# Kernel tuning notes

Hardware: AMD Instinct MI355X
Metric: run time of the kernel (lower is better)

Reference implementation:

```python
import jax, jax.numpy as jnp
import numpy as np

DIM = 768
HEADS = 12
EXPERTS = 8
HID = 3072  # dim * moe_mlp_ratio(=4)
TOP_K = 2
LN_EPS = 1e-5


def _layer_norm(x, g, b):
    mu = x.mean(-1, keepdims=True)
    var = ((x - mu) ** 2).mean(-1, keepdims=True)
    return (x - mu) * jax.lax.rsqrt(var + LN_EPS) * g + b


def setup_inputs() -> dict:
    key = jax.random.key(0)
    ks = jax.random.split(key, 16)
    s = 0.02
    return {
        "x": jax.random.normal(ks[0], (8, 196, DIM), jnp.float32),
        "ln1_g": jnp.ones((DIM,), jnp.float32),
        "ln1_b": jnp.zeros((DIM,), jnp.float32),
        "qkv_w": jax.random.normal(ks[1], (DIM, 3 * DIM), jnp.float32) * s,
        "qkv_b": jnp.zeros((3 * DIM,), jnp.float32),
        "proj_w": jax.random.normal(ks[2], (DIM, DIM), jnp.float32) * s,
        "proj_b": jnp.zeros((DIM,), jnp.float32),
        "ln2_g": jnp.ones((DIM,), jnp.float32),
        "ln2_b": jnp.zeros((DIM,), jnp.float32),
        "gate_w": jax.random.normal(ks[3], (DIM, EXPERTS), jnp.float32) * s,
        "w1": jax.random.normal(ks[4], (EXPERTS, DIM, HID), jnp.float32) * s,
        "b1": jnp.zeros((EXPERTS, HID), jnp.float32),
        "w2": jax.random.normal(ks[5], (EXPERTS, HID, DIM), jnp.float32) * s,
        "b2": jnp.zeros((EXPERTS, DIM), jnp.float32),
    }


def _attention(x, qkv_w, qkv_b, proj_w, proj_b):
    B, N, C = x.shape
    hd = C // HEADS
    qkv = (x @ qkv_w + qkv_b).reshape(B, N, 3, HEADS, hd).transpose(2, 0, 3, 1, 4)
    q, k, v = qkv[0], qkv[1], qkv[2]  # [B,H,N,hd]
    attn = jax.nn.softmax(jnp.einsum("bhnd,bhmd->bhnm", q, k) * (hd ** -0.5), axis=-1)
    o = jnp.einsum("bhnm,bhmd->bhnd", attn, v).transpose(0, 2, 1, 3).reshape(B, N, C)
    return o @ proj_w + proj_b


def _moe_mlp(xn, gate_w, w1, b1, w2, b2):
    # xn: [T, D]; noisy top-k gate in eval mode (no noise)
    T = xn.shape[0]
    logits = xn @ gate_w                                   # [T, E]
    top_logits, top_idx = jax.lax.top_k(logits, TOP_K)     # [T, k]
    top_gates = jax.nn.softmax(top_logits, axis=-1)        # [T, k]
    gates = jnp.zeros((T, EXPERTS), xn.dtype).at[
        jnp.arange(T)[:, None], top_idx
    ].set(top_gates)                                       # [T, E] sparse combine weights
    # dense-masked expert compute (math identical to dispatch: gate=0 tokens contribute 0)
    h = jax.nn.gelu(jnp.einsum("td,edh->teh", xn, w1) + b1, approximate=False)
    y = jnp.einsum("teh,ehd->ted", h, w2) + b2             # [T, E, D]
    return jnp.einsum("ted,te->td", y, gates)


def reference(x, ln1_g, ln1_b, qkv_w, qkv_b, proj_w, proj_b,
              ln2_g, ln2_b, gate_w, w1, b1, w2, b2):
    B, N, C = x.shape
    x = x + _attention(_layer_norm(x, ln1_g, ln1_b), qkv_w, qkv_b, proj_w, proj_b)
    xn = _layer_norm(x, ln2_g, ln2_b).reshape(B * N, C)
    moe_out = _moe_mlp(xn, gate_w, w1, b1, w2, b2).reshape(B, N, C)
    return x + moe_out
```

## Files before the change

### kernel.cpp

```cpp
#include <hip/hip_runtime.h>
#include <hip/hip_bf16.h>
#include <math.h>

#define DIMC 768
#define HEADS 12
#define HD 64
#define EXPERTS 8
#define HID 3072
#define BB 8
#define NN 196
#define TT (BB*NN)
#define CAP_ROWS 4224
#define LN_EPS 1e-5f

typedef float f32x4_t __attribute__((ext_vector_type(4)));
typedef short bf16x8_t __attribute__((ext_vector_type(8)));
typedef unsigned short u16x8_t __attribute__((ext_vector_type(8)));

__device__ __forceinline__ unsigned short f2bf(float f) {
    unsigned int u = __float_as_uint(f);
    u += 0x7FFFu + ((u >> 16) & 1u);
    return (unsigned short)(u >> 16);
}
__device__ __forceinline__ float bf2f(unsigned short u) {
    return __uint_as_float(((unsigned int)u) << 16);
}

__device__ __forceinline__ void gl_lds16(const void* g, void* l) {
    __builtin_amdgcn_global_load_lds(
        (const __attribute__((address_space(1))) unsigned int*)g,
        (__attribute__((address_space(3))) unsigned int*)l, 16, 0, 0);
}

__device__ __forceinline__ int xcd_remap(int pbid, int nwg) {
    int q = nwg >> 3, r8 = nwg & 7;
    int xcd = pbid & 7, slot = pbid >> 3;
    return (xcd < r8) ? xcd * (q + 1) + slot
                      : r8 * (q + 1) + (xcd - r8) * q + slot;
}

template<int GATE>
__global__ void ln_kernel_t(const float* __restrict__ x, const float* __restrict__ g,
                            const float* __restrict__ b,
                            unsigned short* __restrict__ out_hi,
                            unsigned short* __restrict__ out_lo,
                            const float* __restrict__ gw, int* __restrict__ tok_e,
                            float* __restrict__ tok_g, int* __restrict__ counts) {
    int t = blockIdx.x;
    const float* xr = x + (size_t)t * DIMC;
    int tid = threadIdx.x;
    int lane = tid & 63, w = tid >> 6;
    float v0 = xr[tid], v1 = xr[tid + 256], v2 = xr[tid + 512];
    __shared__ float ws[4], vs[4];

    float s = v0 + v1 + v2;
    #pragma unroll
    for (int off = 32; off > 0; off >>= 1) s += __shfl_xor(s, off, 64);
    if (lane == 0) ws[w] = s;
    __syncthreads();
    float mu = (ws[0] + ws[1] + ws[2] + ws[3]) * (1.0f / DIMC);

    float d0 = v0 - mu, d1 = v1 - mu, d2 = v2 - mu;
    float q = d0 * d0 + d1 * d1 + d2 * d2;
    #pragma unroll
    for (int off = 32; off > 0; off >>= 1) q += __shfl_xor(q, off, 64);
    if (lane == 0) vs[w] = q;
    __syncthreads();
    float rstd = rsqrtf((vs[0] + vs[1] + vs[2] + vs[3]) * (1.0f / DIMC) + LN_EPS);

    float o0 = d0 * rstd * g[tid]       + b[tid];
    float o1 = d1 * rstd * g[tid + 256] + b[tid + 256];
    float o2 = d2 * rstd * g[tid + 512] + b[tid + 512];
    {
        unsigned short* o = out_hi + (size_t)t * DIMC;
        unsigned short h0 = f2bf(o0), h1 = f2bf(o1), h2 = f2bf(o2);
        o[tid] = h0; o[tid + 256] = h1; o[tid + 512] = h2;
        if (out_lo) {
            unsigned short* ol = out_lo + (size_t)t * DIMC;
            ol[tid]       = f2bf(o0 - bf2f(h0));
            ol[tid + 256] = f2bf(o1 - bf2f(h1));
            ol[tid + 512] = f2bf(o2 - bf2f(h2));
        }
    }
    if (GATE) {
        float p[8];
        const float* g0r = gw + (size_t)tid * 8;
        const float* g1r = gw + ((size_t)tid + 256) * 8;
        const float* g2r = gw + ((size_t)tid + 512) * 8;
        #pragma unroll
        for (int e = 0; e < 8; ++e)
            p[e] = o0 * g0r[e] + o1 * g1r[e] + o2 * g2r[e];
        #pragma unroll
        for (int off = 32; off > 0; off >>= 1)
            #pragma unroll
            for (int e = 0; e < 8; ++e) p[e] += __shfl_xor(p[e], off, 64);
        __shared__ float redw[4][8];
        if (lane == 0) {
            #pragma unroll
            for (int e = 0; e < 8; ++e) redw[w][e] = p[e];
        }
        __syncthreads();
        if (tid == 0) {
            float lg[8];
            #pragma unroll
            for (int e = 0; e < 8; ++e)
                lg[e] = redw[0][e] + redw[1][e] + redw[2][e] + redw[3][e];
            int e0 = 0; float l0 = lg[0];
            #pragma unroll
            for (int e = 1; e < 8; ++e) if (lg[e] > l0) { l0 = lg[e]; e0 = e; }
            int e1 = -1; float l1 = -3e38f;
            #pragma unroll
            for (int e = 0; e < 8; ++e) if (e != e0 && lg[e] > l1) { l1 = lg[e]; e1 = e; }
            float pp = expf(l1 - l0);
            float ga = 1.f / (1.f + pp);
            float gb = pp / (1.f + pp);
            tok_e[t*2] = e0; tok_e[t*2+1] = e1;
            tok_g[t*2] = ga; tok_g[t*2+1] = gb;
            atomicAdd(&counts[e0], 1);
            atomicAdd(&counts[e1], 1);
        }
    }
}

__global__ void attn_mfma_kernel(const float* __restrict__ qkv,
                                 unsigned short* __restrict__ ao_h,
                                 unsigned short* __restrict__ ao_l) {
    __shared__ char psb[64 * 896];
    __shared__ unsigned short QsH[64 * 64], QsL[64 * 64];
    __shared__ unsigned short KsH[64 * 64], KsL[64 * 64];

    int bh = blockIdx.x;
    int b = bh / HEADS, h = bh % HEADS;
    int q0 = blockIdx.y * 64;
    const float* base = qkv + (size_t)b * NN * 2304 + h * 64;

    int tid = threadIdx.x;
    int sr = tid >> 3, sq = tid & 7;
    int lane = tid & 63;
    int wid = tid >> 6;
    int wm = (wid >> 2) * 32;
    int wn = (wid & 3) * 16;
    int lrow = lane & 15;
    int lq = lane >> 4;
    int colb_base = lq * 16;

    {
        int r = sr;
        int n = q0 + r;
        float v[8] = {0.f,0.f,0.f,0.f,0.f,0.f,0.f,0.f};
        if (n < NN) {
            float4 a0 = *(const float4*)(base + (size_t)n * 2304 + sq * 8);
            float4 a1 = *(const float4*)(base + (size_t)n * 2304 + sq * 8 + 4);
            v[0]=a0.x; v[1]=a0.y; v[2]=a0.z; v[3]=a0.w;
            v[4]=a1.x; v[5]=a1.y; v[6]=a1.z; v[7]=a1.w;
        }
        u16x8_t hv, lv;
        #pragma unroll
        for (int t = 0; t < 8; ++t) {
            unsigned short hh = f2bf(v[t]);
            hv[t] = hh; lv[t] = f2bf(v[t] - bf2f(hh));
        }
        int off = r * 128 + ((sq * 16) ^ ((r & 7) << 4));
        *(u16x8_t*)((char*)QsH + off) = hv;
        *(u16x8_t*)((char*)QsL + off) = lv;
    }

    for (int kt = 0; kt < 4; ++kt) {
        int j0 = kt * 64;
        __syncthreads();
        {
            int r = sr;
            int n = j0 + r;
            float v[8] = {0.f,0.f,0.f,0.f,0.f,0.f,0.f,0.f};
            if (n < NN) {
                float4 a0 = *(const float4*)(base + (size_t)n * 2304 + 768 + sq * 8);
                float4 a1 = *(const float4*)(base + (size_t)n * 2304 + 768 + sq * 8 + 4);
                v[0]=a0.x; v[1]=a0.y; v[2]=a0.z; v[3]=a0.w;
                v[4]=a1.x; v[5]=a1.y; v[6]=a1.z; v[7]=a1.w;
            }
            u16x8_t hv, lv;
            #pragma unroll
            for (int t = 0; t < 8; ++t) {
                unsigned short hh = f2bf(v[t]);
                hv[t] = hh; lv[t] = f2bf(v[t] - bf2f(hh));
            }
            int off = r * 128 + ((sq * 16) ^ ((r & 7) << 4));
            *(u16x8_t*)((char*)KsH + off) = hv;
            *(u16x8_t*)((char*)KsL + off) = lv;
        }
        __syncthreads();

        f32x4_t acc[2] = {};
        #pragma unroll
        for (int kk = 0; kk < 2; ++kk) {
            int colb = kk * 64 + colb_base;
            bf16x8_t qh[2], ql[2], kh, kl;
            #pragma unroll
            for (int i = 0; i < 2; ++i) {
                int ra = wm + i * 16 + lrow;
                int oa = ra * 128 + (colb ^ ((ra & 7) << 4));
                qh[i] = *(const bf16x8_t*)((const char*)QsH + oa);
                ql[i] = *(const bf16x8_t*)((const char*)QsL + oa);
            }
            int rb = wn + lrow;
            int ob = rb * 128 + (colb ^ ((rb & 7) << 4));
            kh = *(const bf16x8_t*)((const char*)KsH + ob);
            kl = *(const bf16x8_t*)((const char*)KsL + ob);
            #pragma unroll
            for (int mi = 0; mi < 2; ++mi) {
                acc[mi] = __builtin_amdgcn_mfma_f32_16x16x32_bf16(qh[mi], kh, acc[mi], 0, 0, 0);
                acc[mi] = __builtin_amdgcn_mfma_f32_16x16x32_bf16(qh[mi], kl, acc[mi], 0, 0, 0);
                acc[mi] = __builtin_amdgcn_mfma_f32_16x16x32_bf16(ql[mi], kh, acc[mi], 0, 0, 0);
            }
        }
        int jc = j0 + wn + lrow;
        if (jc < 224) {
            #pragma unroll
            for (int mi = 0; mi < 2; ++mi) {
                #pragma unroll
                for (int j = 0; j < 4; ++j) {
                    int row = wm + mi * 16 + lq * 4 + j;
                    int s = (row & 7) ^ (row >> 3);
                    *(float*)(psb + row * 896 + ((jc * 4) ^ (s << 4))) = acc[mi][j] * 0.125f;
                }
            }
        }
    }
    __syncthreads();

    {
        int i = tid >> 3, l = tid & 7;
        int s = (i & 7) ^ (i >> 3);
        char* prow = psb + i * 896;
        float mx = -1e30f;
        for (int j = l; j < NN; j += 8) mx = fmaxf(mx, *(const float*)(prow + ((j * 4) ^ (s << 4))));
        mx = fmaxf(mx, __shfl_xor(mx, 1, 8));
        mx = fmaxf(mx, __shfl_xor(mx, 2, 8));
        mx = fmaxf(mx, __shfl_xor(mx, 4, 8));
        float sum = 0.f;
        for (int j = l; j < NN; j += 8) {
            float* pp = (float*)(prow + ((j * 4) ^ (s << 4)));
            float e = expf(*pp - mx); *pp = e; sum += e;
        }
        sum += __shfl_xor(sum, 1, 8);
        sum += __shfl_xor(sum, 2, 8);
        sum += __shfl_xor(sum, 4, 8);
        float inv = 1.f / sum;
        for (int j = l; j < NN; j += 8) {
            float* pp = (float*)(prow + ((j * 4) ^ (s << 4)));
            *pp *= inv;
        }
    }

    f32x4_t oacc[2] = {};
    for (int kt = 0; kt < 4; ++kt) {
        int j0 = kt * 64;
        __syncthreads();
        {
            int r = sr;
            int n = j0 + r;
            float v[8] = {0.f,0.f,0.f,0.f,0.f,0.f,0.f,0.f};
            if (n < NN) {
                float4 a0 = *(const float4*)(base + (size_t)n * 2304 + 1536 + sq * 8);
                float4 a1 = *(const float4*)(base + (size_t)n * 2304 + 1536 + sq * 8 + 4);
                v[0]=a0.x; v[1]=a0.y; v[2]=a0.z; v[3]=a0.w;
                v[4]=a1.x; v[5]=a1.y; v[6]=a1.z; v[7]=a1.w;
            }
            #pragma unroll
            for (int t = 0; t < 8; ++t) {
                int d = sq * 8 + t;
                int sw = ((d & 7) ^ (d >> 3)) << 4;
                unsigned short hh = f2bf(v[t]);
                int off = d * 128 + ((r * 2) ^ sw);
                *(unsigned short*)((char*)KsH + off) = hh;
                *(unsigned short*)((char*)KsL + off) = f2bf(v[t] - bf2f(hh));
            }
        }
        __syncthreads();

        int kkmax = (kt == 3) ? 1 : 2;
        for (int kk = 0; kk < kkmax; ++kk) {
            int colb = kk * 64 + colb_base;
            bf16x8_t pah[2], pal[2], vh, vl;
            #pragma unroll
            for (int i = 0; i < 2; ++i) {
                int ra = wm + i * 16 + lrow;
                int s = (ra & 7) ^ (ra >> 3);
                const char* prow = psb + ra * 896;
                int jb = (j0 + kk * 32 + lq * 8) * 4;
                float4 a0 = *(const float4*)(prow + (jb ^ (s << 4)));
                float4 a1 = *(const float4*)(prow + ((jb + 16) ^ (s << 4)));
                float vv[8] = {a0.x,a0.y,a0.z,a0.w,a1.x,a1.y,a1.z,a1.w};
                u16x8_t hv, lv;
                #pragma unroll
                for (int t = 0; t < 8; ++t) {
                    unsigned short hh = f2bf(vv[t]);
                    hv[t] = hh; lv[t] = f2bf(vv[t] - bf2f(hh));
                }
                pah[i] = *(bf16x8_t*)&hv;
                pal[i] = *(bf16x8_t*)&lv;
            }
            int rb = wn + lrow;
            int ob = rb * 128 + (colb ^ (((rb & 7) ^ (rb >> 3)) << 4));
            vh = *(const bf16x8_t*)((const char*)KsH + ob);
            vl = *(const bf16x8_t*)((const char*)KsL + ob);
            #pragma unroll
            for (int mi = 0; mi < 2; ++mi) {
                oacc[mi] = __builtin_amdgcn_mfma_f32_16x16x32_bf16(pah[mi], vh, oacc[mi], 0, 0, 0);
                oacc[mi] = __builtin_amdgcn_mfma_f32_16x16x32_bf16(pah[mi], vl, oacc[mi], 0, 0, 0);
                oacc[mi] = __builtin_amdgcn_mfma_f32_16x16x32_bf16(pal[mi], vh, oacc[mi], 0, 0, 0);
            }
        }
    }

    #pragma unroll
    for (int mi = 0; mi < 2; ++mi) {
        int col = h * 64 + wn + lrow;
        #pragma unroll
        for (int j = 0; j < 4; ++j) {
            int n = q0 + wm + mi * 16 + lq * 4 + j;
            if (n < NN) {
                float v = oacc[mi][j];
                unsigned short hh = f2bf(v);
                size_t o = (size_t)(b * NN + n) * DIMC + col;
                ao_h[o] = hh;
                ao_l[o] = f2bf(v - bf2f(hh));
            }
        }
    }
}

__global__ void init_kernel(int* __restrict__ counts, int* __restrict__ row2tok, int cap,
                            unsigned short* __restrict__ zrow) {
    int i = blockIdx.x * blockDim.x + threadIdx.x;
    if (i < 8) counts[i] = 0;
    if (i < 128) zrow[i] = 0;
    if (i < cap) row2tok[i] = -1;
}

__global__ void offsets_kernel(const int* __restrict__ counts, int* __restrict__ offsets,
                               int* __restrict__ cursor) {
    if (threadIdx.x == 0 && blockIdx.x == 0) {
        int off = 0;
        for (int e = 0; e < 8; ++e) {
            offsets[e] = off;
            cursor[e]  = off;
            off += ((counts[e] + 127) / 128) * 128;
        }
        offsets[8] = off;
    }
}

__global__ void fill_kernel(const int* __restrict__ tok_e, int* __restrict__ cursor,
                            int* __restrict__ row2tok, int* __restrict__ tok_row) {
    int t = blockIdx.x * blockDim.x + threadIdx.x;
    if (t >= TT) return;
    #pragma unroll
    for (int k = 0; k < 2; ++k) {
        int e = tok_e[t*2+k];
        int slot = atomicAdd(&cursor[e], 1);
        row2tok[slot] = t;
        tok_row[t*2+k] = slot;
    }
}

__global__ void transpose_bf16(const float* __restrict__ src, unsigned short* __restrict__ dst,
                               int R, int C) {
    __shared__ float tile[64][65];
    const float* s = src + (size_t)blockIdx.z * R * C;
    unsigned short* d = dst + (size_t)blockIdx.z * R * C;
    int c0 = blockIdx.x * 64, r0 = blockIdx.y * 64;
    int tid = threadIdx.x;
    int tr = tid >> 4;
    int tc = (tid & 15) * 4;
    #pragma unroll
    for (int p = 0; p < 4; ++p) {
        int r = tr + p * 16;
        const float4 v = *(const float4*)(s + (size_t)(r0 + r) * C + c0 + tc);
        tile[r][tc+0] = v.x; tile[r][tc+1] = v.y; tile[r][tc+2] = v.z; tile[r][tc+3] = v.w;
    }
    __syncthreads();
    #pragma unroll
    for (int p = 0; p < 4; ++p) {
        int c = tr + p * 16;
        ushort4 o;
        o.x = f2bf(tile[tc+0][c]);
        o.y = f2bf(tile[tc+1][c]);
        o.z = f2bf(tile[tc+2][c]);
        o.w = f2bf(tile[tc+3][c]);
        *(ushort4*)(d + (size_t)(c0 + c) * R + r0 + tc) = o;
    }
}

__global__ void transpose_split_bf16(const float* __restrict__ src,
                                     unsigned short* __restrict__ dh,
                                     unsigned short* __restrict__ dl, int R, int C) {
    __shared__ float tile[64][65];
    int c0 = blockIdx.x * 64, r0 = blockIdx.y * 64;
    int tid = threadIdx.x;
    int tr = tid >> 4;
    int tc = (tid & 15) * 4;
    #pragma unroll
    for (int p = 0; p < 4; ++p) {
        int r = tr + p * 16;
        const float4 v = *(const float4*)(src + (size_t)(r0 + r) * C + c0 + tc);
        tile[r][tc+0] = v.x; tile[r][tc+1] = v.y; tile[r][tc+2] = v.z; tile[r][tc+3] = v.w;
    }
    __syncthreads();
    #pragma unroll
    for (int p = 0; p < 4; ++p) {
        int c = tr + p * 16;
        ushort4 h, l;
        float v0 = tile[tc+0][c], v1 = tile[tc+1][c], v2 = tile[tc+2][c], v3 = tile[tc+3][c];
        h.x = f2bf(v0); l.x = f2bf(v0 - bf2f(h.x));
        h.y = f2bf(v1); l.y = f2bf(v1 - bf2f(h.y));
        h.z = f2bf(v2); l.z = f2bf(v2 - bf2f(h.z));
        h.w = f2bf(v3); l.w = f2bf(v3 - bf2f(h.w));
        size_t off = (size_t)(c0 + c) * R + r0 + tc;
        *(ushort4*)(dh + off) = h;
        *(ushort4*)(dl + off) = l;
    }
}

template<int RES>
__global__ void mfma_gemm_split(const unsigned short* __restrict__ Ah,
                                const unsigned short* __restrict__ Al,
                                const unsigned short* __restrict__ Bth,
                                const unsigned short* __restrict__ Btl,
                                const float* __restrict__ bias,
                                const float* __restrict__ res,
                                float* __restrict__ C,
                                const unsigned short* __restrict__ zrow,
                                int M, int N, int K, int nmb) {
    __shared__ unsigned short AsH[64 * 64];
    __shared__ unsigned short AsL[64 * 64];
    __shared__ unsigned short BsH[64 * 64];
    __shared__ unsigned short BsL[64 * 64];

    int L = xcd_remap(blockIdx.x, gridDim.x);
    int m0 = (L % nmb) * 64;
    int n0 = (L / nmb) * 64;
    int tid = threadIdx.x;
    int lane = tid & 63;
    int wid = tid >> 6;
    int wm = (wid >> 1) * 32;
    int wn = (wid & 1) * 32;
    int colb_base = (lane >> 4) * 16;
    int lrow = lane & 15;

    f32x4_t acc[2][2] = {};

    for (int k0 = 0; k0 < K; k0 += 64) {
        #pragma unroll
        for (int p = 0; p < 2; ++p) {
            int s = tid + p * 256;
            int r = s >> 3, c = s & 7;
            int gc = c ^ (r & 7);
            bool inM = (m0 + r < M);
            size_t aoff = (size_t)(m0 + r) * K + k0 + gc * 8;
            gl_lds16(inM ? (const void*)(Ah + aoff) : (const void*)zrow, (char*)AsH + s * 16);
            gl_lds16(inM ? (const void*)(Al + aoff) : (const void*)zrow, (char*)AsL + s * 16);
            size_t boff = (size_t)(n0 + r) * K + k0 + gc * 8;
            gl_lds16((const void*)(Bth + boff), (char*)BsH + s * 16);
            gl_lds16((const void*)(Btl + boff), (char*)BsL + s * 16);
        }
        __syncthreads();
        #pragma unroll
        for (int kk = 0; kk < 2; ++kk) {
            int colb = kk * 64 + colb_base;
            bf16x8_t ah[2], al[2], bh[2], bl[2];
            #pragma unroll
            for (int i = 0; i < 2; ++i) {
                int ra = wm + i * 16 + lrow;
                int oa = ra * 128 + (colb ^ ((ra & 7) << 4));
                ah[i] = *(const bf16x8_t*)((const char*)AsH + oa);
                al[i] = *(const bf16x8_t*)((const char*)AsL + oa);
                int rb = wn + i * 16 + lrow;
                int ob = rb * 128 + (colb ^ ((rb & 7) << 4));
                bh[i] = *(const bf16x8_t*)((const char*)BsH + ob);
                bl[i] = *(const bf16x8_t*)((const char*)BsL + ob);
            }
            #pragma unroll
            for (int mi = 0; mi < 2; ++mi)
                #pragma unroll
                for (int ni = 0; ni < 2; ++ni) {
                    acc[mi][ni] = __builtin_amdgcn_mfma_f32_16x16x32_bf16(
                        ah[mi], bh[ni], acc[mi][ni], 0, 0, 0);
                    acc[mi][ni] = __builtin_amdgcn_mfma_f32_16x16x32_bf16(
                        ah[mi], bl[ni], acc[mi][ni], 0, 0, 0);
                    acc[mi][ni] = __builtin_amdgcn_mfma_f32_16x16x32_bf16(
                        al[mi], bh[ni], acc[mi][ni], 0, 0, 0);
                }
        }
        __syncthreads();
    }

    #pragma unroll
    for (int mi = 0; mi < 2; ++mi) {
        #pragma unroll
        for (int ni = 0; ni < 2; ++ni) {
            int col = n0 + wn + ni * 16 + lrow;
            #pragma unroll
            for (int j = 0; j < 4; ++j) {
                int row = m0 + wm + mi * 16 + (lane >> 4) * 4 + j;
                if (row < M) {
                    float v = acc[mi][ni][j] + bias[col];
                    if (RES) v += res[(size_t)row * N + col];
                    C[(size_t)row * N + col] = v;
                }
            }
        }
    }
}

template<int GATHER, int GELU, int OUT_BF16>
__global__ void mfma_gemm_grouped128(const unsigned short* __restrict__ A,
                                     const unsigned short* __restrict__ Bt,
                                     const float* __restrict__ bias,
                                     const int* __restrict__ offsets,
                                     const int* __restrict__ row2tok,
                                     void* __restrict__ Cout,
                                     const unsigned short* __restrict__ zrow,
                                     int N, int K, int nxb) {
    __shared__ unsigned short As[128 * 64];
    __shared__ unsigned short Bs[128 * 64];
    __shared__ int toks[128];

    int L = xcd_remap(blockIdx.x, gridDim.x);
    int xb = L % nxb;
    int n0 = (L / nxb) * 128;
    int r0 = xb * 128;
    if (r0 >= offsets[8]) return;
    int e = 0;
    while (r0 >= offsets[e + 1]) ++e;

    int tid = threadIdx.x;
    if (GATHER) {
        if (tid < 128) toks[tid] = row2tok[r0 + tid];
        __syncthreads();
    }

    const unsigned short* Be = Bt + (size_t)e * N * K;

    int lane = tid & 63;
    int wid = tid >> 6;
    int wm = (wid >> 1) * 64;
    int wn = (wid & 1) * 64;
    int colb_base = (lane >> 4) * 16;
    int lrow = lane & 15;

    f32x4_t acc[4][4] = {};

    for (int k0 = 0; k0 < K; k0 += 64) {
        #pragma unroll
        for (int p = 0; p < 4; ++p) {
            int s = tid + p * 256;
            int r = s >> 3, c = s & 7;
            int gc = c ^ (r & 7);
            const void* asrc;
            if (GATHER) {
                int tok = toks[r];
                asrc = (tok >= 0) ? (const void*)(A + (size_t)tok * K + k0 + gc * 8)
                                  : (const void*)zrow;
            } else {
                asrc = (const void*)(A + (size_t)(r0 + r) * K + k0 + gc * 8);
            }
            gl_lds16(asrc, (char*)As + s * 16);
            gl_lds16((const void*)(Be + (size_t)(n0 + r) * K + k0 + gc * 8),
                     (char*)Bs + s * 16);
        }
        __syncthreads();
        #pragma unroll
        for (int kk = 0; kk < 2; ++kk) {
            int colb = kk * 64 + colb_base;
            bf16x8_t a[4], b[4];
            #pragma unroll
            for (int i = 0; i < 4; ++i) {
                int ra = wm + i * 16 + lrow;
                a[i] = *(const bf16x8_t*)((const char*)As + ra * 128 + (colb ^ ((ra & 7) << 4)));
                int rb = wn + i * 16 + lrow;
                b[i] = *(const bf16x8_t*)((const char*)Bs + rb * 128 + (colb ^ ((rb & 7) << 4)));
            }
            #pragma unroll
            for (int mi = 0; mi < 4; ++mi)
                #pragma unroll
                for (int ni = 0; ni < 4; ++ni)
                    acc[mi][ni] = __builtin_amdgcn_mfma_f32_16x16x32_bf16(
                        a[mi], b[ni], acc[mi][ni], 0, 0, 0);
        }
        __syncthreads();
    }

    #pragma unroll
    for (int mi = 0; mi < 4; ++mi) {
        #pragma unroll
        for (int ni = 0; ni < 4; ++ni) {
            int col = n0 + wn + ni * 16 + lrow;
            float bv = GELU ? bias[(size_t)e * N + col] : 0.f;
            #pragma unroll
            for (int j = 0; j < 4; ++j) {
                int row = r0 + wm + mi * 16 + (lane >> 4) * 4 + j;
                float v = acc[mi][ni][j] + bv;
                if (GELU) v = 0.5f * v * (1.f + erff(v * 0.70710678f));
                if (OUT_BF16)
                    ((unsigned short*)Cout)[(size_t)row * N + col] = f2bf(v);
                else
                    ((float*)Cout)[(size_t)row * N + col] = v;
            }
        }
    }
}

template<int GATHER, int GELU, int OUT_BF16>
__global__ void mfma_gemm_grouped(const unsigned short* __restrict__ A,
                                  const unsigned short* __restrict__ Bt,
                                  const float* __restrict__ bias,
                                  const int* __restrict__ offsets,
                                  const int* __restrict__ row2tok,
                                  void* __restrict__ Cout,
                                  const unsigned short* __restrict__ zrow,
                                  int N, int K, int nxb) {
    __shared__ unsigned short As[64 * 128];
    __shared__ unsigned short Bs[128 * 128];
    __shared__ int toks[64];

    int L = xcd_remap(blockIdx.x, gridDim.x);
    int xb = L % nxb;
    int n0 = (L / nxb) * 128;
    int r0 = xb * 64;
    if (r0 >= offsets[8]) return;
    int e = 0;
    while (r0 >= offsets[e + 1]) ++e;

    int tid = threadIdx.x;
    if (GATHER && tid < 64) toks[tid] = row2tok[r0 + tid];
    __syncthreads();

    const unsigned short* Be = Bt + (size_t)e * N * K;

    int lane = tid & 63;
    int wid = tid >> 6;
    int wm = (wid >> 1) * 32;
    int wn = (wid & 1) * 64;
    int colb_base = (lane >> 4) * 16;
    int lrow = lane & 15;

    f32x4_t acc[2][4] = {};

    for (int k0 = 0; k0 < K; k0 += 128) {
        #pragma unroll
        for (int p = 0; p < 4; ++p) {
            int s = tid + p * 256;
            int r = s >> 4, c = s & 15;
            int gc = c ^ (r & 7);
            const void* asrc;
            if (GATHER) {
                int tok = toks[r];
                asrc = (tok >= 0) ? (const void*)(A + (size_t)tok * K + k0 + gc * 8)
                                  : (const void*)zrow;
            } else {
                asrc = (const void*)(A + (size_t)(r0 + r) * K + k0 + gc * 8);
            }
            gl_lds16(asrc, (char*)As + s * 16);
        }
        #pragma unroll
        for (int p = 0; p < 8; ++p) {
            int s = tid + p * 256;
            int r = s >> 4, c = s & 15;
            int gc = c ^ (r & 7);
            gl_lds16((const void*)(Be + (size_t)(n0 + r) * K + k0 + gc * 8),
                     (char*)Bs + s * 16);
        }
        __syncthreads();
        #pragma unroll
        for (int kk = 0; kk < 4; ++kk) {
            int colb = kk * 64 + colb_base;
            bf16x8_t a[2], b[4];
            #pragma unroll
            for (int i = 0; i < 2; ++i) {
                int ra = wm + i * 16 + lrow;
                a[i] = *(const bf16x8_t*)((const char*)As + ra * 256 + (colb ^ ((ra & 7) << 4)));
            }
            #pragma unroll
            for (int i = 0; i < 4; ++i) {
                int rb = wn + i * 16 + lrow;
                b[i] = *(const bf16x8_t*)((const char*)Bs + rb * 256 + (colb ^ ((rb & 7) << 4)));
            }
            #pragma unroll
            for (int mi = 0; mi < 2; ++mi)
                #pragma unroll
                for (int ni = 0; ni < 4; ++ni)
                    acc[mi][ni] = __builtin_amdgcn_mfma_f32_16x16x32_bf16(
                        a[mi], b[ni], acc[mi][ni], 0, 0, 0);
        }
        __syncthreads();
    }

    #pragma unroll
    for (int mi = 0; mi < 2; ++mi) {
        #pragma unroll
        for (int ni = 0; ni < 4; ++ni) {
            int col = n0 + wn + ni * 16 + lrow;
            float bv = GELU ? bias[(size_t)e * N + col] : 0.f;
            #pragma unroll
            for (int j = 0; j < 4; ++j) {
                int row = r0 + wm + mi * 16 + (lane >> 4) * 4 + j;
                float v = acc[mi][ni][j] + bv;
                if (GELU) v = 0.5f * v * (1.f + erff(v * 0.70710678f));
                if (OUT_BF16)
                    ((unsigned short*)Cout)[(size_t)row * N + col] = f2bf(v);
                else
                    ((float*)Cout)[(size_t)row * N + col] = v;
            }
        }
    }
}

__global__ void combine_kernel(const float* __restrict__ x_res, const float* __restrict__ y,
                               const float* __restrict__ b2, const int* __restrict__ tok_e,
                               const float* __restrict__ tok_g, const int* __restrict__ tok_row,
                               float* __restrict__ out) {
    int t = blockIdx.x;
    int c = blockIdx.y * 256 + threadIdx.x;
    int e0 = tok_e[t*2], e1 = tok_e[t*2+1];
    float g0 = tok_g[t*2], g1 = tok_g[t*2+1];
    int r0 = tok_row[t*2], r1 = tok_row[t*2+1];
    float v = x_res[(size_t)t * DIMC + c]
            + g0 * (y[(size_t)r0 * DIMC + c] + b2[(size_t)e0 * DIMC + c])
            + g1 * (y[(size_t)r1 * DIMC + c] + b2[(size_t)e1 * DIMC + c]);
    out[(size_t)t * DIMC + c] = v;
}

extern "C" void kernel_launch(void* const* d_in, const int* in_sizes, int n_in,
                              void* d_out, int out_size, void* d_ws, size_t ws_size,
                              hipStream_t stream) {
    const float* x      = (const float*)d_in[0];
    const float* ln1_g  = (const float*)d_in[1];
    const float* ln1_b  = (const float*)d_in[2];
    const float* qkv_w  = (const float*)d_in[3];
    const float* qkv_b  = (const float*)d_in[4];
    const float* proj_w = (const float*)d_in[5];
    const float* proj_b = (const float*)d_in[6];
    const float* ln2_g  = (const float*)d_in[7];
    const float* ln2_b  = (const float*)d_in[8];
    const float* gate_w = (const float*)d_in[9];
    const float* w1     = (const float*)d_in[10];
    const float* b1     = (const float*)d_in[11];
    const float* w2     = (const float*)d_in[12];
    const float* b2     = (const float*)d_in[13];
    float* out = (float*)d_out;

    char* p = (char*)d_ws;
    auto alloc = [&](size_t nbytes) {
        void* r = (void*)p;
        p += (nbytes + 255) & ~(size_t)255;
        return r;
    };
    unsigned short* xn1_h   = (unsigned short*)alloc((size_t)TT * DIMC * 2);
    unsigned short* xn1_l   = (unsigned short*)alloc((size_t)TT * DIMC * 2);
    float*          qkv     = (float*)alloc((size_t)TT * 2304 * 4);
    unsigned short* ao_h    = (unsigned short*)alloc((size_t)TT * DIMC * 2);
    unsigned short* ao_l    = (unsigned short*)alloc((size_t)TT * DIMC * 2);
    float*          x_res   = (float*)alloc((size_t)TT * DIMC * 4);
    unsigned short* xn2_bf  = (unsigned short*)alloc((size_t)TT * DIMC * 2);
    unsigned short* h       = (unsigned short*)alloc((size_t)CAP_ROWS * HID * 2);
    float*          y       = (float*)alloc((size_t)CAP_ROWS * DIMC * 4);
    unsigned short* w1t     = (unsigned short*)alloc((size_t)EXPERTS * DIMC * HID * 2);
    unsigned short* w2t     = (unsigned short*)alloc((size_t)EXPERTS * DIMC * HID * 2);
    unsigned short* qwt_h   = (unsigned short*)alloc((size_t)DIMC * 2304 * 2);
    unsigned short* qwt_l   = (unsigned short*)alloc((size_t)DIMC * 2304 * 2);
    unsigned short* pwt_h   = (unsigned short*)alloc((size_t)DIMC * DIMC * 2);
    unsigned short* pwt_l   = (unsigned short*)alloc((size_t)DIMC * DIMC * 2);
    float*          tok_g   = (float*)alloc((size_t)2 * TT * 4);
    int*            tok_e   = (int*)alloc((size_t)2 * TT * 4);
    int*            tok_row = (int*)alloc((size_t)2 * TT * 4);
    int*            row2tok = (int*)alloc((size_t)CAP_ROWS * 4);
    unsigned short* zrow    = (unsigned short*)alloc(256);
    int*            counts  = (int*)alloc(32 * 4);
    int*            offsets = (int*)alloc(32 * 4);
    int*            cursor  = (int*)alloc(32 * 4);

    init_kernel<<<(CAP_ROWS + 255) / 256, 256, 0, stream>>>(counts, row2tok, CAP_ROWS, zrow);

    transpose_bf16<<<dim3(HID / 64, DIMC / 64, EXPERTS), 256, 0, stream>>>(w1, w1t, DIMC, HID);
    transpose_bf16<<<dim3(DIMC / 64, HID / 64, EXPERTS), 256, 0, stream>>>(w2, w2t, HID, DIMC);
    transpose_split_bf16<<<dim3(2304 / 64, DIMC / 64), 256, 0, stream>>>(qkv_w, qwt_h, qwt_l,
                                                                         DIMC, 2304);
    transpose_split_bf16<<<dim3(DIMC / 64, DIMC / 64), 256, 0, stream>>>(proj_w, pwt_h, pwt_l,
                                                                         DIMC, DIMC);

    ln_kernel_t<0><<<TT, 256, 0, stream>>>(x, ln1_g, ln1_b, xn1_h, xn1_l,
                                           nullptr, nullptr, nullptr, nullptr);

    {
        int nmb = (TT + 63) / 64;
        int nwg = nmb * (2304 / 64);
        mfma_gemm_split<0><<<nwg, 256, 0, stream>>>(
            xn1_h, xn1_l, qwt_h, qwt_l, qkv_b, nullptr, qkv, zrow, TT, 2304, DIMC, nmb);
    }

    attn_mfma_kernel<<<dim3(BB * HEADS, 4), 512, 0, stream>>>(qkv, ao_h, ao_l);

    {
        int nmb = (TT + 63) / 64;
        int nwg = nmb * (DIMC / 64);
        mfma_gemm_split<1><<<nwg, 256, 0, stream>>>(
            ao_h, ao_l, pwt_h, pwt_l, proj_b, x, x_res, zrow, TT, DIMC, DIMC, nmb);
    }

    ln_kernel_t<1><<<TT, 256, 0, stream>>>(x_res, ln2_g, ln2_b, xn2_bf, nullptr,
                                           gate_w, tok_e, tok_g, counts);

    offsets_kernel<<<1, 64, 0, stream>>>(counts, offsets, cursor);

    fill_kernel<<<(TT + 255) / 256, 256, 0, stream>>>(tok_e, cursor, row2tok, tok_row);

    {
        int nxb1 = CAP_ROWS / 128;
        int nwg1 = (HID / 128) * nxb1;
        mfma_gemm_grouped128<1, 1, 1><<<nwg1, 256, 0, stream>>>(
            xn2_bf, w1t, b1, offsets, row2tok, h, zrow, HID, DIMC, nxb1);

        int nxb2 = CAP_ROWS / 64;
        int nwg2 = (DIMC / 128) * nxb2;
        mfma_gemm_grouped<0, 0, 0><<<nwg2, 256, 0, stream>>>(
            h, w2t, nullptr, offsets, row2tok, y, zrow, DIMC, HID, nxb2);
    }

    combine_kernel<<<dim3(TT, 3), 256, 0, stream>>>(x_res, y, b2, tok_e, tok_g, tok_row, out);
}
```

Baseline: 265.6 us.

## Fuse expert weight transpose and bf16 cast into grouped GEMM B-tile loads

Drops the two standalone transpose_bf16 launches for the expert weights w1 and w2. The grouped GEMMs now read fp32 weights directly with float4 loads, convert them to bf16 in registers, and write pairs of k values into a shared-memory tile. The tile uses a new XOR swizzle to limit bank conflicts. This removes a full pass over the expert weights plus two launches, but each GEMM workgroup now re-reads fp32 weights (twice the bytes of bf16) and does conversion ALU work and scalar LDS stores instead of async direct-to-LDS loads.

```diff
diff --git a/kernel.cpp b/kernel.cpp
--- a/kernel.cpp
+++ b/kernel.cpp
@@ -364,34 +364,6 @@
     }
 }
 
-__global__ void transpose_bf16(const float* __restrict__ src, unsigned short* __restrict__ dst,
-                               int R, int C) {
-    __shared__ float tile[64][65];
-    const float* s = src + (size_t)blockIdx.z * R * C;
-    unsigned short* d = dst + (size_t)blockIdx.z * R * C;
-    int c0 = blockIdx.x * 64, r0 = blockIdx.y * 64;
-    int tid = threadIdx.x;
-    int tr = tid >> 4;
-    int tc = (tid & 15) * 4;
-    #pragma unroll
-    for (int p = 0; p < 4; ++p) {
-        int r = tr + p * 16;
-        const float4 v = *(const float4*)(s + (size_t)(r0 + r) * C + c0 + tc);
-        tile[r][tc+0] = v.x; tile[r][tc+1] = v.y; tile[r][tc+2] = v.z; tile[r][tc+3] = v.w;
-    }
-    __syncthreads();
-    #pragma unroll
-    for (int p = 0; p < 4; ++p) {
-        int c = tr + p * 16;
-        ushort4 o;
-        o.x = f2bf(tile[tc+0][c]);
-        o.y = f2bf(tile[tc+1][c]);
-        o.z = f2bf(tile[tc+2][c]);
-        o.w = f2bf(tile[tc+3][c]);
-        *(ushort4*)(d + (size_t)(c0 + c) * R + r0 + tc) = o;
-    }
-}
-
 __global__ void transpose_split_bf16(const float* __restrict__ src,
                                      unsigned short* __restrict__ dh,
                                      unsigned short* __restrict__ dl, int R, int C) {
@@ -515,7 +487,7 @@
 
 template<int GATHER, int GELU, int OUT_BF16>
 __global__ void mfma_gemm_grouped128(const unsigned short* __restrict__ A,
-                                     const unsigned short* __restrict__ Bt,
+                                     const float* __restrict__ W,
                                      const float* __restrict__ bias,
                                      const int* __restrict__ offsets,
                                      const int* __restrict__ row2tok,
@@ -540,7 +512,7 @@
         __syncthreads();
     }
 
-    const unsigned short* Be = Bt + (size_t)e * N * K;
+    const float* We = W + (size_t)e * K * N;
 
     int lane = tid & 63;
     int wid = tid >> 6;
@@ -566,8 +538,25 @@
                 asrc = (const void*)(A + (size_t)(r0 + r) * K + k0 + gc * 8);
             }
             gl_lds16(asrc, (char*)As + s * 16);
-            gl_lds16((const void*)(Be + (size_t)(n0 + r) * K + k0 + gc * 8),
-                     (char*)Bs + s * 16);
+        }
+        #pragma unroll
+        for (int p = 0; p < 4; ++p) {
+            int idx = tid + p * 256;
+            int nc = idx & 31;
+            int k2 = idx >> 5;
+            const float* w0 = We + (size_t)(k0 + 2 * k2) * N + n0 + nc * 4;
+            float4 a = *(const float4*)w0;
+            float4 bq = *(const float4*)(w0 + N);
+            float av[4] = {a.x, a.y, a.z, a.w};
+            float bv[4] = {bq.x, bq.y, bq.z, bq.w};
+            #pragma unroll
+            for (int j = 0; j < 4; ++j) {
+                int n = nc * 4 + j;
+                int sw = (((n & 7) ^ ((n >> 3) & 7)) << 4);
+                unsigned int pk = (unsigned int)f2bf(av[j]) |
+                                  ((unsigned int)f2bf(bv[j]) << 16);
+                *(unsigned int*)((char*)Bs + n * 128 + ((k2 * 4) ^ sw)) = pk;
+            }
         }
         __syncthreads();
         #pragma unroll
@@ -579,7 +568,8 @@
                 int ra = wm + i * 16 + lrow;
                 a[i] = *(const bf16x8_t*)((const char*)As + ra * 128 + (colb ^ ((ra & 7) << 4)));
                 int rb = wn + i * 16 + lrow;
-                b[i] = *(const bf16x8_t*)((const char*)Bs + rb * 128 + (colb ^ ((rb & 7) << 4)));
+                int sb = (((rb & 7) ^ ((rb >> 3) & 7)) << 4);
+                b[i] = *(const bf16x8_t*)((const char*)Bs + rb * 128 + (colb ^ sb));
             }
             #pragma unroll
             for (int mi = 0; mi < 4; ++mi)
@@ -613,7 +603,7 @@
 
 template<int GATHER, int GELU, int OUT_BF16>
 __global__ void mfma_gemm_grouped(const unsigned short* __restrict__ A,
-                                  const unsigned short* __restrict__ Bt,
+                                  const float* __restrict__ W,
                                   const float* __restrict__ bias,
                                   const int* __restrict__ offsets,
                                   const int* __restrict__ row2tok,
@@ -636,7 +626,7 @@
     if (GATHER && tid < 64) toks[tid] = row2tok[r0 + tid];
     __syncthreads();
 
-    const unsigned short* Be = Bt + (size_t)e * N * K;
+    const float* We = W + (size_t)e * K * N;
 
     int lane = tid & 63;
     int wid = tid >> 6;
@@ -665,11 +655,22 @@
         }
         #pragma unroll
         for (int p = 0; p < 8; ++p) {
-            int s = tid + p * 256;
-            int r = s >> 4, c = s & 15;
-            int gc = c ^ (r & 7);
-            gl_lds16((const void*)(Be + (size_t)(n0 + r) * K + k0 + gc * 8),
-                     (char*)Bs + s * 16);
+            int idx = tid + p * 256;
+            int nc = idx & 31;
+            int k2 = idx >> 5;
+            const float* w0 = We + (size_t)(k0 + 2 * k2) * N + n0 + nc * 4;
+            float4 a = *(const float4*)w0;
+            float4 bq = *(const float4*)(w0 + N);
+            float av[4] = {a.x, a.y, a.z, a.w};
+            float bv[4] = {bq.x, bq.y, bq.z, bq.w};
+            #pragma unroll
+            for (int j = 0; j < 4; ++j) {
+                int n = nc * 4 + j;
+                int sw = (((n & 7) ^ ((n >> 3) & 7)) << 4);
+                unsigned int pk = (unsigned int)f2bf(av[j]) |
+                                  ((unsigned int)f2bf(bv[j]) << 16);
+                *(unsigned int*)((char*)Bs + n * 256 + ((k2 * 4) ^ sw)) = pk;
+            }
         }
         __syncthreads();
         #pragma unroll
@@ -684,7 +685,8 @@
             #pragma unroll
             for (int i = 0; i < 4; ++i) {
                 int rb = wn + i * 16 + lrow;
-                b[i] = *(const bf16x8_t*)((const char*)Bs + rb * 256 + (colb ^ ((rb & 7) << 4)));
+                int sb = (((rb & 7) ^ ((rb >> 3) & 7)) << 4);
+                b[i] = *(const bf16x8_t*)((const char*)Bs + rb * 256 + (colb ^ sb));
             }
             #pragma unroll
             for (int mi = 0; mi < 2; ++mi)
@@ -765,8 +767,6 @@
     unsigned short* xn2_bf  = (unsigned short*)alloc((size_t)TT * DIMC * 2);
     unsigned short* h       = (unsigned short*)alloc((size_t)CAP_ROWS * HID * 2);
     float*          y       = (float*)alloc((size_t)CAP_ROWS * DIMC * 4);
-    unsigned short* w1t     = (unsigned short*)alloc((size_t)EXPERTS * DIMC * HID * 2);
-    unsigned short* w2t     = (unsigned short*)alloc((size_t)EXPERTS * DIMC * HID * 2);
     unsigned short* qwt_h   = (unsigned short*)alloc((size_t)DIMC * 2304 * 2);
     unsigned short* qwt_l   = (unsigned short*)alloc((size_t)DIMC * 2304 * 2);
     unsigned short* pwt_h   = (unsigned short*)alloc((size_t)DIMC * DIMC * 2);
@@ -782,8 +782,6 @@
 
     init_kernel<<<(CAP_ROWS + 255) / 256, 256, 0, stream>>>(counts, row2tok, CAP_ROWS, zrow);
 
-    transpose_bf16<<<dim3(HID / 64, DIMC / 64, EXPERTS), 256, 0, stream>>>(w1, w1t, DIMC, HID);
-    transpose_bf16<<<dim3(DIMC / 64, HID / 64, EXPERTS), 256, 0, stream>>>(w2, w2t, HID, DIMC);
     transpose_split_bf16<<<dim3(2304 / 64, DIMC / 64), 256, 0, stream>>>(qkv_w, qwt_h, qwt_l,
                                                                          DIMC, 2304);
     transpose_split_bf16<<<dim3(DIMC / 64, DIMC / 64), 256, 0, stream>>>(proj_w, pwt_h, pwt_l,
@@ -819,12 +817,12 @@
         int nxb1 = CAP_ROWS / 128;
         int nwg1 = (HID / 128) * nxb1;
         mfma_gemm_grouped128<1, 1, 1><<<nwg1, 256, 0, stream>>>(
-            xn2_bf, w1t, b1, offsets, row2tok, h, zrow, HID, DIMC, nxb1);
+            xn2_bf, w1, b1, offsets, row2tok, h, zrow, HID, DIMC, nxb1);
 
         int nxb2 = CAP_ROWS / 64;
         int nwg2 = (DIMC / 128) * nxb2;
         mfma_gemm_grouped<0, 0, 0><<<nwg2, 256, 0, stream>>>(
-            h, w2t, nullptr, offsets, row2tok, y, zrow, DIMC, HID, nxb2);
+            h, w2, nullptr, offsets, row2tok, y, zrow, DIMC, HID, nxb2);
     }
 
     combine_kernel<<<dim3(TT, 3), 256, 0, stream>>>(x_res, y, b2, tok_e, tok_g, tok_row, out);
```

After: 490.4 us. 84.7% more time.
